# Kernel tuning notes

Hardware: AMD Instinct MI355X
Metric: run time of the kernel (lower is better)

## Reference

```python
import jax, jax.numpy as jnp
import numpy as np

K = 4            # number of modes (init kwarg)
ALPHA = 2000.0   # bandwidth constraint
TAU = 0.0        # dual ascent step (0 -> exact reconstruction slack)
N_ITERS = 20     # fixed ADMM iterations (orig: tol-based while loop, max 500)


def vmd_batch(x):
    # x: [B, C, T] float32 -> (u: [B, C, K, T], omega: [B, C, K])
    B, C, T = x.shape
    T2 = 2 * T
    half = T2 // 2
    # mirror extension (vmdpy): flip first half | signal | flip second half
    f = jnp.concatenate([x[..., :T // 2][..., ::-1], x, x[..., T // 2:][..., ::-1]], axis=-1)  # [B,C,T2]
    t = jnp.arange(1, T2 + 1, dtype=jnp.float32) / T2
    freqs = t - 0.5 - 1.0 / T2                       # [T2], centered frequency axis
    freqs_pos = freqs[half:]                          # [T], positive frequencies
    f_hat = jnp.fft.fftshift(jnp.fft.fft(f, axis=-1), axes=-1).astype(jnp.complex64)
    f_hat_plus = f_hat.at[..., :half].set(0.0)        # keep analytic (positive-freq) part
    # init=1: uniform initial center frequencies
    omega = jnp.broadcast_to((0.5 / K) * jnp.arange(K, dtype=jnp.float32), (B, C, K))
    u_hat = jnp.zeros((B, C, K, T2), dtype=jnp.complex64)
    lam = jnp.zeros((B, C, T2), dtype=jnp.complex64)  # dual variable lambda_hat

    def step(carry, _):
        u_hat, omega, lam = carry
        S = jnp.sum(u_hat, axis=2)                    # running sum of all modes [B,C,T2]
        new_u, new_w = [], []
        for k in range(K):                            # Gauss-Seidel sweep over K modes (K small, unrolled)
            S = S - u_hat[:, :, k]                    # sum of all other modes (updated ones included)
            denom = 1.0 + ALPHA * (freqs[None, None, :] - omega[:, :, k:k + 1]) ** 2
            uk = (f_hat_plus - S + lam / 2.0) / denom # Wiener-filter spectral update [B,C,T2]
            S = S + uk
            p = uk.real[..., half:] ** 2 + uk.imag[..., half:] ** 2  # power on positive freqs [B,C,T]
            wk = jnp.sum(freqs_pos * p, axis=-1) / jnp.sum(p, axis=-1)  # center-frequency re-estimate
            new_u.append(uk)
            new_w.append(wk)
        u_hat = jnp.stack(new_u, axis=2)
        omega = jnp.stack(new_w, axis=-1)
        lam = lam + TAU * (S - f_hat_plus)            # dual ascent (tau=0 -> no-op, kept for fidelity)
        return (u_hat, omega, lam), None

    (u_hat, omega, lam), _ = jax.lax.scan(step, (u_hat, omega, lam), None, length=N_ITERS)

    # reconstruct full conjugate-symmetric spectrum
    pos = u_hat[..., half:]                           # [B,C,K,T]
    full = jnp.zeros((B, C, K, T2), dtype=jnp.complex64)
    full = full.at[..., half:].set(pos)
    full = full.at[..., 1:half + 1].set(jnp.conj(pos)[..., ::-1])  # full[half-j] = conj(pos[j])
    full = full.at[..., 0].set(jnp.conj(full[..., -1]))
    u = jnp.real(jnp.fft.ifft(jnp.fft.ifftshift(full, axes=-1), axis=-1))  # [B,C,K,T2]
    u = u[..., T2 // 4: 3 * T2 // 4]                  # de-mirror: center T samples
    return u, omega


def setup_inputs() -> dict:
    key = jax.random.key(0)
    x = jax.random.normal(key, (16, 8192, 4), dtype=jnp.float32)  # [B, T, C]
    return {"x": x}


def reference(x):
    # module forward: permute [B,T,C] -> [B,C,T], run VMD, return u:[B,K,T,C], omega:[B,K]
    u, omega = vmd_batch(jnp.transpose(x, (0, 2, 1)))
    u = jnp.transpose(u, (0, 2, 3, 1))                # [B,K,T,C]
    omega_b = jnp.mean(omega, axis=1)                 # collapse channel dim -> [B,K]
    return (u, omega_b)
```

## Files before the change

### kernel.cpp

```cpp
#include <hip/hip_runtime.h>


#define HALF      8192
#define NH        8192
#define NTHREADS  1024
#define KMODES    4
#define NITERS    20
#define ALPHA_F   2000.0f
#define SQH       0.70710678118654752440f
#define NSPLIT    4
#define SENTINEL  0xFFFFFFFFu

typedef __fp16 half2_t __attribute__((ext_vector_type(2)));
typedef float  v2f     __attribute__((ext_vector_type(2)));

__device__ __forceinline__ unsigned bitrev13(unsigned x) { return __brev(x) >> 19; }
__device__ __forceinline__ int pidx(int i) { return i + (i >> 4); }

__device__ __forceinline__ unsigned pack_h2(float a, float b) {
    half2_t h = __builtin_amdgcn_cvt_pkrtz(a, b);
    return __builtin_bit_cast(unsigned, h);
}
__device__ __forceinline__ v2f unpack_h2(unsigned u) {
    half2_t h = __builtin_bit_cast(half2_t, u);
    v2f r; r.x = (float)h.x; r.y = (float)h.y; return r;
}

template <int CTRL>
__device__ __forceinline__ float dpp_add_step(float v) {
    int r = __builtin_amdgcn_update_dpp(0, __float_as_int(v), CTRL, 0xf, 0xf, true);
    return v + __int_as_float(r);
}
__device__ __forceinline__ float wave64_sum(float v) {
    v = dpp_add_step<0x111>(v);
    v = dpp_add_step<0x112>(v);
    v = dpp_add_step<0x114>(v);
    v = dpp_add_step<0x118>(v);
    v = dpp_add_step<0x142>(v);
    v = dpp_add_step<0x143>(v);
    return v;
}

__device__ __forceinline__ float2 cmul(float2 a, float wr, float wi) {
    return make_float2(a.x * wr - a.y * wi, a.x * wi + a.y * wr);
}
__device__ __forceinline__ float2 cadd(float2 a, float2 b) {
    return make_float2(a.x + b.x, a.y + b.y);
}
__device__ __forceinline__ float2 csub(float2 a, float2 b) {
    return make_float2(a.x - b.x, a.y - b.y);
}

template <bool INV>
__device__ __forceinline__ void fft_pass8(float2* A, int tid, int t) {
    const int   log2Q = 10 - 3 * t;
    const int   Q     = 1 << log2Q;
    const float invL  = (float)(1 << (3 * t)) * (1.0f / 8192.0f);
    const int j    = tid & (Q - 1);
    const int base = ((tid >> log2Q) << (log2Q + 3)) + j;

    float2 x[8];
    #pragma unroll
    for (int m = 0; m < 8; ++m) x[m] = A[pidx(base + m * Q)];

    float rev = (float)j * invL;
    float w1r = __builtin_amdgcn_cosf(rev);
    float w1i = INV ?  __builtin_amdgcn_sinf(rev)
                    : -__builtin_amdgcn_sinf(rev);
    float w2r = w1r * w1r - w1i * w1i, w2i = 2.0f * w1r * w1i;
    float w4r = w2r * w2r - w2i * w2i, w4i = 2.0f * w2r * w2i;
    float wsr, wsi;
    if (INV) { wsr = SQH * (w1r - w1i); wsi = SQH * (w1r + w1i); }
    else     { wsr = SQH * (w1r + w1i); wsi = SQH * (w1i - w1r); }
    float w1tr = INV ? -w1i : w1i,  w1ti = INV ? w1r : -w1r;
    float wstr = INV ? -wsi : wsi,  wsti = INV ? wsr : -wsr;
    float w2tr = INV ? -w2i : w2i,  w2ti = INV ? w2r : -w2r;

    float2 y0 = cadd(x[0], x[4]), y1 = cadd(x[1], x[5]);
    float2 y2 = cadd(x[2], x[6]), y3 = cadd(x[3], x[7]);
    float2 y4 = cmul(csub(x[0], x[4]), w1r, w1i);
    float2 y5 = cmul(csub(x[1], x[5]), wsr, wsi);
    float2 y6 = cmul(csub(x[2], x[6]), w1tr, w1ti);
    float2 y7 = cmul(csub(x[3], x[7]), wstr, wsti);

    float2 z0 = cadd(y0, y2), z2 = cmul(csub(y0, y2), w2r, w2i);
    float2 z1 = cadd(y1, y3), z3 = cmul(csub(y1, y3), w2tr, w2ti);
    float2 z4 = cadd(y4, y6), z6 = cmul(csub(y4, y6), w2r, w2i);
    float2 z5 = cadd(y5, y7), z7 = cmul(csub(y5, y7), w2tr, w2ti);

    A[pidx(base + 0 * Q)] = cadd(z0, z1);
    A[pidx(base + 1 * Q)] = cmul(csub(z0, z1), w4r, w4i);
    A[pidx(base + 2 * Q)] = cadd(z2, z3);
    A[pidx(base + 3 * Q)] = cmul(csub(z2, z3), w4r, w4i);
    A[pidx(base + 4 * Q)] = cadd(z4, z5);
    A[pidx(base + 5 * Q)] = cmul(csub(z4, z5), w4r, w4i);
    A[pidx(base + 6 * Q)] = cadd(z6, z7);
    A[pidx(base + 7 * Q)] = cmul(csub(z6, z7), w4r, w4i);
}

__device__ __forceinline__ void fft_last2(float2* A, int tid) {
    #pragma unroll
    for (int u = 0; u < 4; ++u) {
        int t  = tid + u * NTHREADS;
        int i0 = 2 * t, i1 = 2 * t + 1;
        float2 a = A[pidx(i0)], b = A[pidx(i1)];
        A[pidx(i0)] = make_float2(a.x + b.x, a.y + b.y);
        A[pidx(i1)] = make_float2(a.x - b.x, a.y - b.y);
    }
}

__device__ __forceinline__ int mirror_t(int i) {
    if (i < 4096)       return 4095 - i;
    else if (i < 12288) return i - 4096;
    else                return 20479 - i;
}

__global__ __launch_bounds__(NTHREADS) void vmd_forward_iter(
    const float* __restrict__ x, unsigned* __restrict__ ws_u,
    float* __restrict__ ws_omega, unsigned* __restrict__ ws_part)
{
    __shared__ float2 A[NH + (NH >> 4)];
    const int tid = threadIdx.x;
    const int bid = blockIdx.x;
    const int ch  = bid & 63;
    const int q   = bid >> 6;
    const int b   = ch >> 2, c = ch & 3;
    const float* xb = x + (size_t)b * 8192 * 4 + c;

    for (int m = tid; m < NH; m += NTHREADS) {
        float re = xb[(size_t)mirror_t(2 * m) * 4];
        float im = xb[(size_t)mirror_t(2 * m + 1) * 4];
        A[pidx(m)] = make_float2(re, im);
    }
    __syncthreads();

    for (int t = 0; t < 4; ++t) {
        fft_pass8<false>(A, tid, t);
        __syncthreads();
    }
    fft_last2(A, tid);
    __syncthreads();

    v2f R[2];
    #pragma unroll
    for (int u = 0; u < 2; ++u) {
        int j  = (q << 11) + tid + u * NTHREADS;
        float2 z1 = A[pidx((int)bitrev13((unsigned)j))];
        float2 z2 = A[pidx((int)bitrev13((unsigned)((NH - j) & (NH - 1))))];
        float ex = 0.5f * (z1.x + z2.x);
        float ey = 0.5f * (z1.y - z2.y);
        float dx = 0.5f * (z1.x - z2.x);
        float dy = 0.5f * (z1.y + z2.y);
        float rev = (float)j * (1.0f / 16384.0f);
        float wr = __builtin_amdgcn_cosf(rev);
        float wi = -__builtin_amdgcn_sinf(rev);
        R[u].x = ex + wr * dy + wi * dx;
        R[u].y = ey + wi * dy - wr * dx;
    }
    __syncthreads();

    v2f Up[KMODES][2];
    #pragma unroll
    for (int u = 0; u < 2; ++u)
        #pragma unroll
        for (int k = 0; k < KMODES; ++k) { Up[k][u].x = 0.f; Up[k][u].y = 0.f; }

    const float f0 = (float)((q << 11) + tid) * (1.0f / 16384.0f);
    float omg[KMODES] = {0.0f, 0.125f, 0.25f, 0.375f};

    float* red = (float*)A;
    const int lane = tid & 63, wid = tid >> 6;

    for (int it = 0; it < NITERS; ++it) {
        v2f nd[KMODES];
        #pragma unroll
        for (int k = 0; k < KMODES; ++k) { nd[k].x = 0.f; nd[k].y = 0.f; }
        #pragma unroll
        for (int u = 0; u < 2; ++u) {
            const float fru = f0 + (float)u * 0.0625f;
            v2f fv; fv.x = fru; fv.y = 1.0f;
            #pragma unroll
            for (int k = 0; k < KMODES; ++k) {
                float d   = fru - omg[k];
                float dnm = fmaf(ALPHA_F * d, d, 1.0f);
                float rcp = __builtin_amdgcn_rcpf(dnm);
                v2f uo  = Up[k][u];
                v2f nm  = R[u] + uo;
                v2f un  = nm * rcp;
                R[u]    = nm - un;
                Up[k][u] = un;
                float p = fmaf(un.x, un.x, un.y * un.y);
                nd[k]   = fv * p + nd[k];
            }
        }
        float num[KMODES], den[KMODES];
        #pragma unroll
        for (int m = 0; m < KMODES; ++m) {
            num[m] = wave64_sum(nd[m].x);
            den[m] = wave64_sum(nd[m].y);
        }
        float* redb = red + (it & 1) * 144;
        if (lane == 63) {
            float4* r4 = (float4*)&redb[wid * 8];
            r4[0] = make_float4(num[0], num[1], num[2], num[3]);
            r4[1] = make_float4(den[0], den[1], den[2], den[3]);
        }
        __syncthreads();
        const bool last_it = (it == NITERS - 1);
        unsigned* pp = ws_part + (((size_t)it * 64 + ch) << 5);
        if (wid == 0) {
            float v = redb[lane] + redb[lane + 64];
            v += __int_as_float(__builtin_amdgcn_ds_swizzle(__float_as_int(v), 0x201F));
            v += __int_as_float(__builtin_amdgcn_ds_swizzle(__float_as_int(v), 0x401F));
            v += __int_as_float(__builtin_amdgcn_ds_bpermute((lane ^ 32) << 2,
                                                             __float_as_int(v)));
            if (lane < 8)
                __hip_atomic_store(pp + (q << 3) + lane, __float_as_uint(v),
                                   __ATOMIC_RELAXED, __HIP_MEMORY_SCOPE_AGENT);
            if (!last_it || q == 0) {
                float t = 0.0f;
                if (lane < 32) {
                    unsigned w;
                    for (;;) {
                        w = __hip_atomic_load(pp + lane, __ATOMIC_RELAXED,
                                              __HIP_MEMORY_SCOPE_AGENT);
                        if (w != SENTINEL) break;
                        __builtin_amdgcn_s_sleep(1);
                    }
                    t = __uint_as_float(w);
                }
                t += __int_as_float(__builtin_amdgcn_ds_swizzle(__float_as_int(t), 0x201F));
                t += __int_as_float(__builtin_amdgcn_ds_swizzle(__float_as_int(t), 0x401F));
                if (!last_it) {
                    if (lane < 8) redb[128 + lane] = t;
                } else {
                    #pragma unroll
                    for (int m = 0; m < KMODES; ++m) {
                        float nm_ = __int_as_float(__builtin_amdgcn_readlane(__float_as_int(t), m));
                        float dn_ = __int_as_float(__builtin_amdgcn_readlane(__float_as_int(t), m + 4));
                        omg[m] = nm_ * __builtin_amdgcn_rcpf(dn_);
                    }
                }
            }
        }
        if (!last_it) {
            __syncthreads();
            #pragma unroll
            for (int m = 0; m < KMODES; ++m) {
                float nm_ = redb[128 + m];
                float dn_ = redb[128 + m + 4];
                omg[m] = nm_ * __builtin_amdgcn_rcpf(dn_);
            }
        }
    }

    #pragma unroll
    for (int k = 0; k < KMODES; ++k) {
        unsigned* dst = ws_u + (size_t)(ch * KMODES + k) * HALF + (q << 11);
        #pragma unroll
        for (int u = 0; u < 2; ++u)
            dst[tid + u * NTHREADS] = pack_h2(Up[k][u].x, Up[k][u].y);
    }
    if (q == 0 && tid < KMODES) ws_omega[ch * KMODES + tid] = omg[tid];
}

__global__ __launch_bounds__(NTHREADS) void vmd_inverse(
    const unsigned* __restrict__ ws_u, const float* __restrict__ ws_omega,
    float* __restrict__ out)
{
    __shared__ float2 A[NH + (NH >> 4)];
    const int tid = threadIdx.x;
    const int bid = blockIdx.x;
    const int g   = bid & 63;
    const int c   = bid >> 6;
    const int b   = g >> 2, k = g & 3;
    const int ch  = b * 4 + c;
    const unsigned* pos = ws_u + (size_t)(ch * KMODES + k) * HALF;

    if (bid == 0 && tid < 64) {
        int bb = tid >> 2, kk = tid & 3;
        float s = 0.f;
        #pragma unroll
        for (int cc = 0; cc < 4; ++cc) s += ws_omega[(bb * 4 + cc) * 4 + kk];
        out[2097152 + tid] = 0.25f * s;
    }

    for (int j = tid; j < NH; j += NTHREADS) {
        v2f pj = unpack_h2(pos[j]);
        v2f ph = unpack_h2(pos[j ? (HALF - j) : (HALF - 1)]);
        float gjx = pj.x, gjy = (j == 0) ? -pj.y : pj.y;
        float ghx = ph.x, ghy = -ph.y;
        float ex = 0.5f * (gjx + ghx), ey = 0.5f * (gjy + ghy);
        float dx = 0.5f * (gjx - ghx), dy = 0.5f * (gjy - ghy);
        float rev = (float)j * (1.0f / 16384.0f);
        float wr = __builtin_amdgcn_cosf(rev);
        float wi = __builtin_amdgcn_sinf(rev);
        float ox = dx * wr - dy * wi;
        float oy = dx * wi + dy * wr;
        A[pidx(j)] = make_float2(ex - oy, ey + ox);
    }
    __syncthreads();

    for (int t = 0; t < 4; ++t) {
        fft_pass8<true>(A, tid, t);
        __syncthreads();
    }
    fft_last2(A, tid);
    __syncthreads();

    float* outp = out + (size_t)(b * 4 + k) * 8192 * 4 + c;
    for (int m = 2048 + tid; m < 6144; m += NTHREADS) {
        float2 z = A[pidx((int)bitrev13((unsigned)m))];
        int t0 = 2 * m - 4096;
        outp[(size_t)t0 * 4]       = z.x * (1.0f / 8192.0f);
        outp[(size_t)(t0 + 1) * 4] = z.y * (1.0f / 8192.0f);
    }
}

extern "C" void kernel_launch(void* const* d_in, const int* in_sizes, int n_in,
                              void* d_out, int out_size, void* d_ws, size_t ws_size,
                              hipStream_t stream)
{
    (void)in_sizes; (void)n_in; (void)out_size; (void)ws_size;
    const float* x = (const float*)d_in[0];
    float* out = (float*)d_out;

    unsigned* ws_u     = (unsigned*)d_ws;
    float*    ws_omega = (float*)((char*)d_ws + (size_t)64 * 4 * HALF * 4);
    unsigned* ws_part  = (unsigned*)((char*)d_ws + (size_t)64 * 4 * HALF * 4 + 1024);

    hipMemsetAsync(ws_part, 0xFF, (size_t)NITERS * 64 * 32 * 4, stream);
    vmd_forward_iter<<<256, NTHREADS, 0, stream>>>(x, ws_u, ws_omega, ws_part);
    vmd_inverse<<<256, NTHREADS, 0, stream>>>(ws_u, ws_omega, out);
}
```

Baseline: 89.12 us.

## Fuse forward iteration and inverse FFT kernels with device-scope completion flags

Merges the forward ADMM kernel and the inverse-FFT kernel into one launch. Each block publishes its slice of the mode spectra and omega, then sets a per-channel done flag; the inverse phase spin-waits on the four flags of the channel it needs instead of relying on a kernel boundary. This removes one kernel launch and its drain/fill gap. In exchange it adds global spin-waits and relaxed atomic loads for the spectrum reads, and it relies on all 256 blocks being co-resident to avoid deadlock.

```diff
diff --git a/kernel.cpp b/kernel.cpp
--- a/kernel.cpp
+++ b/kernel.cpp
@@ -8,7 +8,6 @@
 #define NITERS    20
 #define ALPHA_F   2000.0f
 #define SQH       0.70710678118654752440f
-#define NSPLIT    4
 #define SENTINEL  0xFFFFFFFFu
 
 typedef __fp16 half2_t __attribute__((ext_vector_type(2)));
@@ -24,6 +23,13 @@
 __device__ __forceinline__ v2f unpack_h2(unsigned u) {
     half2_t h = __builtin_bit_cast(half2_t, u);
     v2f r; r.x = (float)h.x; r.y = (float)h.y; return r;
+}
+
+__device__ __forceinline__ unsigned ic_load(const unsigned* p) {
+    return __hip_atomic_load(p, __ATOMIC_RELAXED, __HIP_MEMORY_SCOPE_AGENT);
+}
+__device__ __forceinline__ void ic_store(unsigned* p, unsigned v) {
+    __hip_atomic_store(p, v, __ATOMIC_RELAXED, __HIP_MEMORY_SCOPE_AGENT);
 }
 
 template <int CTRL>
@@ -115,9 +121,10 @@
     else                return 20479 - i;
 }
 
-__global__ __launch_bounds__(NTHREADS) void vmd_forward_iter(
+__global__ __launch_bounds__(NTHREADS) void vmd_fused(
     const float* __restrict__ x, unsigned* __restrict__ ws_u,
-    float* __restrict__ ws_omega, unsigned* __restrict__ ws_part)
+    unsigned* __restrict__ ws_omega, unsigned* __restrict__ ws_part,
+    unsigned* __restrict__ ws_udone, float* __restrict__ out)
 {
     __shared__ float2 A[NH + (NH >> 4)];
     const int tid = threadIdx.x;
@@ -215,15 +222,13 @@
             v += __int_as_float(__builtin_amdgcn_ds_bpermute((lane ^ 32) << 2,
                                                              __float_as_int(v)));
             if (lane < 8)
-                __hip_atomic_store(pp + (q << 3) + lane, __float_as_uint(v),
-                                   __ATOMIC_RELAXED, __HIP_MEMORY_SCOPE_AGENT);
+                ic_store(pp + (q << 3) + lane, __float_as_uint(v));
             if (!last_it || q == 0) {
                 float t = 0.0f;
                 if (lane < 32) {
                     unsigned w;
                     for (;;) {
-                        w = __hip_atomic_load(pp + lane, __ATOMIC_RELAXED,
-                                              __HIP_MEMORY_SCOPE_AGENT);
+                        w = ic_load(pp + lane);
                         if (w != SENTINEL) break;
                         __builtin_amdgcn_s_sleep(1);
                     }
@@ -259,45 +264,72 @@
         unsigned* dst = ws_u + (size_t)(ch * KMODES + k) * HALF + (q << 11);
         #pragma unroll
         for (int u = 0; u < 2; ++u)
-            dst[tid + u * NTHREADS] = pack_h2(Up[k][u].x, Up[k][u].y);
-    }
-    if (q == 0 && tid < KMODES) ws_omega[ch * KMODES + tid] = omg[tid];
-}
-
-__global__ __launch_bounds__(NTHREADS) void vmd_inverse(
-    const unsigned* __restrict__ ws_u, const float* __restrict__ ws_omega,
-    float* __restrict__ out)
-{
-    __shared__ float2 A[NH + (NH >> 4)];
-    const int tid = threadIdx.x;
-    const int bid = blockIdx.x;
-    const int g   = bid & 63;
-    const int c   = bid >> 6;
-    const int b   = g >> 2, k = g & 3;
-    const int ch  = b * 4 + c;
-    const unsigned* pos = ws_u + (size_t)(ch * KMODES + k) * HALF;
+            ic_store(dst + tid + u * NTHREADS, pack_h2(Up[k][u].x, Up[k][u].y));
+    }
+    if (q == 0 && tid < KMODES)
+        ic_store(ws_omega + ch * KMODES + tid, __float_as_uint(omg[tid]));
+    asm volatile("s_waitcnt vmcnt(0)" ::: "memory");
+    __syncthreads();
+    if (tid == 0)
+        ic_store(ws_udone + (ch << 2) + q, 0u);
+
+    const int g2  = bid & 63;
+    const int c2  = bid >> 6;
+    const int b2  = g2 >> 2, k2 = g2 & 3;
+    const int ch2 = b2 * 4 + c2;
+    const unsigned* pos = ws_u + (size_t)(ch2 * KMODES + k2) * HALF;
 
     if (bid == 0 && tid < 64) {
         int bb = tid >> 2, kk = tid & 3;
         float s = 0.f;
         #pragma unroll
-        for (int cc = 0; cc < 4; ++cc) s += ws_omega[(bb * 4 + cc) * 4 + kk];
+        for (int cc = 0; cc < 4; ++cc) {
+            const unsigned* p = ws_omega + ((bb * 4 + cc) << 2) + kk;
+            unsigned w;
+            for (;;) {
+                w = ic_load(p);
+                if (w != SENTINEL) break;
+                __builtin_amdgcn_s_sleep(1);
+            }
+            s += __uint_as_float(w);
+        }
         out[2097152 + tid] = 0.25f * s;
     }
 
-    for (int j = tid; j < NH; j += NTHREADS) {
-        v2f pj = unpack_h2(pos[j]);
-        v2f ph = unpack_h2(pos[j ? (HALF - j) : (HALF - 1)]);
-        float gjx = pj.x, gjy = (j == 0) ? -pj.y : pj.y;
-        float ghx = ph.x, ghy = -ph.y;
-        float ex = 0.5f * (gjx + ghx), ey = 0.5f * (gjy + ghy);
-        float dx = 0.5f * (gjx - ghx), dy = 0.5f * (gjy - ghy);
-        float rev = (float)j * (1.0f / 16384.0f);
-        float wr = __builtin_amdgcn_cosf(rev);
-        float wi = __builtin_amdgcn_sinf(rev);
-        float ox = dx * wr - dy * wi;
-        float oy = dx * wi + dy * wr;
-        A[pidx(j)] = make_float2(ex - oy, ey + ox);
+    if (tid < 4) {
+        const unsigned* p = ws_udone + (ch2 << 2) + tid;
+        for (;;) {
+            unsigned w = ic_load(p);
+            if (w != SENTINEL) break;
+            __builtin_amdgcn_s_sleep(1);
+        }
+    }
+    __syncthreads();
+
+    {
+        unsigned wj[8], wh[8];
+        #pragma unroll
+        for (int uu = 0; uu < 8; ++uu) {
+            int j = tid + uu * NTHREADS;
+            wj[uu] = ic_load(pos + j);
+            wh[uu] = ic_load(pos + (j ? (HALF - j) : (HALF - 1)));
+        }
+        #pragma unroll
+        for (int uu = 0; uu < 8; ++uu) {
+            int j = tid + uu * NTHREADS;
+            v2f pj = unpack_h2(wj[uu]);
+            v2f ph = unpack_h2(wh[uu]);
+            float gjx = pj.x, gjy = (j == 0) ? -pj.y : pj.y;
+            float ghx = ph.x, ghy = -ph.y;
+            float ex = 0.5f * (gjx + ghx), ey = 0.5f * (gjy + ghy);
+            float dx = 0.5f * (gjx - ghx), dy = 0.5f * (gjy - ghy);
+            float rev = (float)j * (1.0f / 16384.0f);
+            float wr = __builtin_amdgcn_cosf(rev);
+            float wi = __builtin_amdgcn_sinf(rev);
+            float ox = dx * wr - dy * wi;
+            float oy = dx * wi + dy * wr;
+            A[pidx(j)] = make_float2(ex - oy, ey + ox);
+        }
     }
     __syncthreads();
 
@@ -308,7 +340,7 @@
     fft_last2(A, tid);
     __syncthreads();
 
-    float* outp = out + (size_t)(b * 4 + k) * 8192 * 4 + c;
+    float* outp = out + (size_t)(b2 * 4 + k2) * 8192 * 4 + c2;
     for (int m = 2048 + tid; m < 6144; m += NTHREADS) {
         float2 z = A[pidx((int)bitrev13((unsigned)m))];
         int t0 = 2 * m - 4096;
@@ -326,10 +358,12 @@
     float* out = (float*)d_out;
 
     unsigned* ws_u     = (unsigned*)d_ws;
-    float*    ws_omega = (float*)((char*)d_ws + (size_t)64 * 4 * HALF * 4);
-    unsigned* ws_part  = (unsigned*)((char*)d_ws + (size_t)64 * 4 * HALF * 4 + 1024);
-
-    hipMemsetAsync(ws_part, 0xFF, (size_t)NITERS * 64 * 32 * 4, stream);
-    vmd_forward_iter<<<256, NTHREADS, 0, stream>>>(x, ws_u, ws_omega, ws_part);
-    vmd_inverse<<<256, NTHREADS, 0, stream>>>(ws_u, ws_omega, out);
-}
+    unsigned* ws_omega = (unsigned*)((char*)d_ws + (size_t)64 * 4 * HALF * 4);
+    unsigned* ws_part  = ws_omega + 256;
+    unsigned* ws_udone = ws_part + (size_t)NITERS * 64 * 32;
+
+    hipMemsetAsync(ws_omega, 0xFF,
+                   (size_t)(256 + NITERS * 64 * 32 + 256) * 4, stream);
+    vmd_fused<<<256, NTHREADS, 0, stream>>>(x, ws_u, ws_omega, ws_part,
+                                            ws_udone, out);
+}
```

Result: faster. 84.61 us (-5.1%).

## Split forward FFT and ADMM iterations into separate kernels

Applied to the files above, without the earlier changes.

Splits the fused forward kernel into an FFT kernel that writes the analytic spectrum to a workspace, and an iteration kernel that only needs a small shared reduction buffer. The iteration kernel, which spin-waits on cross-block partial sums, no longer reserves the large FFT shared array, so its blocks can be co-resident with less LDS pressure. In exchange it adds a kernel launch and a global-memory round trip for the spectrum.

```diff
diff --git a/kernel.cpp b/kernel.cpp
--- a/kernel.cpp
+++ b/kernel.cpp
@@ -8,7 +8,6 @@
 #define NITERS    20
 #define ALPHA_F   2000.0f
 #define SQH       0.70710678118654752440f
-#define NSPLIT    4
 #define SENTINEL  0xFFFFFFFFu
 
 typedef __fp16 half2_t __attribute__((ext_vector_type(2)));
@@ -115,9 +114,8 @@
     else                return 20479 - i;
 }
 
-__global__ __launch_bounds__(NTHREADS) void vmd_forward_iter(
-    const float* __restrict__ x, unsigned* __restrict__ ws_u,
-    float* __restrict__ ws_omega, unsigned* __restrict__ ws_part)
+__global__ __launch_bounds__(NTHREADS) void vmd_fft(
+    const float* __restrict__ x, float2* __restrict__ ws_R)
 {
     __shared__ float2 A[NH + (NH >> 4)];
     const int tid = threadIdx.x;
@@ -141,7 +139,6 @@
     fft_last2(A, tid);
     __syncthreads();
 
-    v2f R[2];
     #pragma unroll
     for (int u = 0; u < 2; ++u) {
         int j  = (q << 11) + tid + u * NTHREADS;
@@ -154,10 +151,27 @@
         float rev = (float)j * (1.0f / 16384.0f);
         float wr = __builtin_amdgcn_cosf(rev);
         float wi = -__builtin_amdgcn_sinf(rev);
-        R[u].x = ex + wr * dy + wi * dx;
-        R[u].y = ey + wi * dy - wr * dx;
-    }
-    __syncthreads();
+        ws_R[(size_t)bid * 2048 + tid + u * NTHREADS] =
+            make_float2(ex + wr * dy + wi * dx, ey + wi * dy - wr * dx);
+    }
+}
+
+__global__ __launch_bounds__(NTHREADS) void vmd_iter(
+    const float2* __restrict__ ws_R, unsigned* __restrict__ ws_u,
+    float* __restrict__ ws_omega, unsigned* __restrict__ ws_part)
+{
+    __shared__ float red[2 * 144];
+    const int tid = threadIdx.x;
+    const int bid = blockIdx.x;
+    const int ch  = bid & 63;
+    const int q   = bid >> 6;
+
+    v2f R[2];
+    #pragma unroll
+    for (int u = 0; u < 2; ++u) {
+        float2 r = ws_R[(size_t)bid * 2048 + tid + u * NTHREADS];
+        R[u].x = r.x; R[u].y = r.y;
+    }
 
     v2f Up[KMODES][2];
     #pragma unroll
@@ -168,7 +182,6 @@
     const float f0 = (float)((q << 11) + tid) * (1.0f / 16384.0f);
     float omg[KMODES] = {0.0f, 0.125f, 0.25f, 0.375f};
 
-    float* red = (float*)A;
     const int lane = tid & 63, wid = tid >> 6;
 
     for (int it = 0; it < NITERS; ++it) {
@@ -328,8 +341,11 @@
     unsigned* ws_u     = (unsigned*)d_ws;
     float*    ws_omega = (float*)((char*)d_ws + (size_t)64 * 4 * HALF * 4);
     unsigned* ws_part  = (unsigned*)((char*)d_ws + (size_t)64 * 4 * HALF * 4 + 1024);
+    float2*   ws_R     = (float2*)((char*)d_ws + (size_t)64 * 4 * HALF * 4 + 1024
+                                   + (size_t)NITERS * 64 * 32 * 4);
 
     hipMemsetAsync(ws_part, 0xFF, (size_t)NITERS * 64 * 32 * 4, stream);
-    vmd_forward_iter<<<256, NTHREADS, 0, stream>>>(x, ws_u, ws_omega, ws_part);
+    vmd_fft<<<256, NTHREADS, 0, stream>>>(x, ws_R);
+    vmd_iter<<<256, NTHREADS, 0, stream>>>(ws_R, ws_u, ws_omega, ws_part);
     vmd_inverse<<<256, NTHREADS, 0, stream>>>(ws_u, ws_omega, out);
 }
```

After: 98.15 us. 10.1% more time.
